# Optimization experiments

Measured on AMD Instinct MI355X. Metric: run time of the kernel, lower is better.

Reference implementation:

```python
import jax, jax.numpy as jnp
import numpy as np

D_MODEL = 2048
N_HEADS = 16
HEAD_DIM = D_MODEL // N_HEADS
B, T = 4, 2048


def setup_inputs() -> dict:
    key = jax.random.key(0)
    ks = jax.random.split(key, 10)
    s = 1.0 / np.sqrt(D_MODEL)
    x = jax.random.normal(ks[0], (B, T, D_MODEL), dtype=jnp.float32)
    # causal additive mask, broadcastable to [B, H, T, T]
    neg = jnp.finfo(jnp.float32).min
    causal = jnp.triu(jnp.full((T, T), neg, dtype=jnp.float32), k=1)
    mask = causal[None, None, :, :]
    return {
        "x": x,
        "mask": mask,
        "Wq": jax.random.uniform(ks[1], (D_MODEL, D_MODEL), jnp.float32, -s, s),
        "bq": jax.random.uniform(ks[2], (D_MODEL,), jnp.float32, -s, s),
        "Wk": jax.random.uniform(ks[3], (D_MODEL, HEAD_DIM), jnp.float32, -s, s),
        "bk": jax.random.uniform(ks[4], (HEAD_DIM,), jnp.float32, -s, s),
        "Wv": jax.random.uniform(ks[5], (D_MODEL, HEAD_DIM), jnp.float32, -s, s),
        "bv": jax.random.uniform(ks[6], (HEAD_DIM,), jnp.float32, -s, s),
        "Wo": jax.random.uniform(ks[7], (D_MODEL, D_MODEL), jnp.float32, -s, s),
        "bo": jax.random.uniform(ks[8], (D_MODEL,), jnp.float32, -s, s),
    }


def reference(x, mask, Wq, bq, Wk, bk, Wv, bv, Wo, bo):
    Bb, Tt, _ = x.shape
    H, Dh = N_HEADS, HEAD_DIM
    scale = 1.0 / jnp.sqrt(jnp.float32(Dh))
    q = (x @ Wq + bq).reshape(Bb, Tt, H, Dh)          # [B,T,H,D]
    k = x @ Wk + bk                                    # [B,T,D] (single KV head)
    v = x @ Wv + bv                                    # [B,T,D]
    # scores: [B,H,T,T] — q heads against shared k
    attn = jnp.einsum("bthd,bsd->bhts", q, k) * scale
    attn = attn + mask
    attn = jax.nn.softmax(attn, axis=-1)
    out = jnp.einsum("bhts,bsd->bthd", attn, v).reshape(Bb, Tt, D_MODEL)
    return out @ Wo + bo
```

## Files before the change

### kernel.cpp

```cpp
#include <hip/hip_runtime.h>
#include <hip/hip_bf16.h>
#include <stdint.h>

#define DEV __device__ __forceinline__

typedef unsigned short u16;
typedef unsigned int u32;
typedef __bf16 bf16x8 __attribute__((ext_vector_type(8)));
typedef float f32x4 __attribute__((ext_vector_type(4)));
typedef u16 u16x4 __attribute__((ext_vector_type(4)));
typedef u32 u32x2 __attribute__((ext_vector_type(2)));
typedef u32 u32x4 __attribute__((ext_vector_type(4)));

typedef __attribute__((address_space(1))) u32 u32_as1;
typedef __attribute__((address_space(3))) u32 u32_as3;

static constexpr int Bn = 4, Tn = 2048, Dm = 2048, Hn = 16, Dh = 128;
static constexpr int BT = Bn * Tn;
static constexpr int KVSTR = 256;

#define VMCNT(n) asm volatile("s_waitcnt vmcnt(" #n ")" ::: "memory")
#define BARRIER() __builtin_amdgcn_s_barrier()

DEV u16 f2bf(float f) {
  u32 u = __builtin_bit_cast(u32, f);
  u += 0x7fffu + ((u >> 16) & 1u);
  return (u16)(u >> 16);
}
DEV u16 cvt_bf(float f) { return __builtin_bit_cast(u16, (__bf16)f); }
DEV u32 cvt_pk_bf16(float lo, float hi) {
  u32 r;
  asm("v_cvt_pk_bf16_f32 %0, %1, %2" : "=v"(r) : "v"(lo), "v"(hi));
  return r;
}

DEV void gl2lds16(const void* g, void* l) {
  __builtin_amdgcn_global_load_lds((u32_as1*)(uintptr_t)g,
                                   (u32_as3*)(u32)(uintptr_t)l, 16, 0, 0);
}

__global__ __launch_bounds__(256) void k_cast_bf16(const float* __restrict__ in,
                                                   u16* __restrict__ out, int n4) {
  int i = blockIdx.x * 256 + threadIdx.x;
  int stride = gridDim.x * 256;
  for (; i < n4; i += stride) {
    f32x4 v = ((const f32x4*)in)[i];
    u16x4 o;
    o.x = f2bf(v.x); o.y = f2bf(v.y); o.z = f2bf(v.z); o.w = f2bf(v.w);
    ((u16x4*)out)[i] = o;
  }
}

__global__ __launch_bounds__(256) void k_transpose_cast(const float* __restrict__ in,
                                                        u16* __restrict__ out,
                                                        int R, int C) {
  __shared__ float t[32][33];
  const int r0 = blockIdx.y * 32, c0 = blockIdx.x * 32;
  const int x = threadIdx.x, y = threadIdx.y;
#pragma unroll
  for (int i = 0; i < 4; ++i)
    t[y + i * 8][x] = in[(size_t)(r0 + y + i * 8) * C + c0 + x];
  __syncthreads();
#pragma unroll
  for (int i = 0; i < 4; ++i)
    out[(size_t)(c0 + y + i * 8) * R + r0 + x] = f2bf(t[x][y + i * 8]);
}

__global__ __launch_bounds__(256) void k_transpose_bf16(const u16* __restrict__ in,
                                                        int inStride,
                                                        u16* __restrict__ out,
                                                        int R, int C) {
  __shared__ u16 t[32][34];
  const int r0 = blockIdx.y * 32, c0 = blockIdx.x * 32;
  const int x = threadIdx.x, y = threadIdx.y;
#pragma unroll
  for (int i = 0; i < 4; ++i)
    t[y + i * 8][x] = in[(size_t)(r0 + y + i * 8) * inStride + c0 + x];
  __syncthreads();
#pragma unroll
  for (int i = 0; i < 4; ++i)
    out[(size_t)(c0 + y + i * 8) * R + r0 + x] = t[x][y + i * 8];
}

__global__ void k_concat_bias(const float* __restrict__ a, const float* __restrict__ b,
                              float* __restrict__ dst) {
  int i = threadIdx.x;
  dst[i] = (i < 128) ? a[i] : b[i - 128];
}

template <typename OutT>
__global__ __launch_bounds__(256) void k_gemm_bt(const u16* __restrict__ A,
                                                 const u16* __restrict__ Bt,
                                                 const float* __restrict__ bias,
                                                 OutT* __restrict__ C,
                                                 int M, int N, int K) {
  __shared__ __align__(128) char smem[32768];
  char* As = smem;
  char* Bs = smem + 16384;
  const int tid = threadIdx.x;
  const int wid = tid >> 6, lane = tid & 63;
  const int g = lane >> 4, r = lane & 15;
  const int wr = wid >> 1, wc = wid & 1;
  const int m0 = blockIdx.x * 128, n0 = blockIdx.y * 128;

  f32x4 acc[4][4];
#pragma unroll
  for (int m = 0; m < 4; ++m)
#pragma unroll
    for (int n = 0; n < 4; ++n) acc[m][n] = (f32x4)(0.f);

  for (int k0 = 0; k0 < K; k0 += 64) {
#pragma unroll
    for (int n = 0; n < 4; ++n) {
      const int L = n * 4096 + tid * 16;
      const int row = L >> 7;
      const int colb = (L & 127) ^ ((row & 7) << 4);
      gl2lds16((const char*)A + ((size_t)(m0 + row) * K + k0) * 2 + colb, As + L);
      gl2lds16((const char*)Bt + ((size_t)(n0 + row) * K + k0) * 2 + colb, Bs + L);
    }
    __syncthreads();
#pragma unroll
    for (int kk = 0; kk < 2; ++kk) {
      bf16x8 a[4], b[4];
#pragma unroll
      for (int m = 0; m < 4; ++m) {
        const int row = wr * 64 + m * 16 + r;
        a[m] = *(const bf16x8*)(As + row * 128 + ((kk * 64 + g * 16) ^ ((row & 7) << 4)));
      }
#pragma unroll
      for (int n = 0; n < 4; ++n) {
        const int row = wc * 64 + n * 16 + r;
        b[n] = *(const bf16x8*)(Bs + row * 128 + ((kk * 64 + g * 16) ^ ((row & 7) << 4)));
      }
#pragma unroll
      for (int m = 0; m < 4; ++m)
#pragma unroll
        for (int n = 0; n < 4; ++n)
          acc[m][n] = __builtin_amdgcn_mfma_f32_16x16x32_bf16(a[m], b[n], acc[m][n], 0, 0, 0);
    }
    __syncthreads();
  }

#pragma unroll
  for (int n = 0; n < 4; ++n) {
    const int col = n0 + wc * 64 + n * 16 + r;
    const float bv = bias[col];
#pragma unroll
    for (int m = 0; m < 4; ++m) {
#pragma unroll
      for (int j = 0; j < 4; ++j) {
        const int grow = m0 + wr * 64 + m * 16 + 4 * g + j;
        const float v = acc[m][n][j] + bv;
        if constexpr (sizeof(OutT) == 2)
          ((u16*)C)[(size_t)grow * N + col] = f2bf(v);
        else
          ((float*)C)[(size_t)grow * N + col] = v;
      }
    }
  }
}

template <typename OutT>
__global__ __launch_bounds__(512, 2) void k_gemm256(const u16* __restrict__ A,
                                                    const u16* __restrict__ Bt,
                                                    const float* __restrict__ bias,
                                                    OutT* __restrict__ C,
                                                    int M, int N, int K) {
  extern __shared__ char smem[];
  const int tid = threadIdx.x;
  const int wid = tid >> 6, lane = tid & 63;
  const int g = lane >> 4, r = lane & 15;
  const int wm = wid >> 2, wn = wid & 3;

  const int nbn = N >> 8;
  const int cpx = gridDim.x >> 3;
  const int linear = (blockIdx.x & 7) * cpx + (blockIdx.x >> 3);
  const int m0 = (linear / nbn) << 8;
  const int n0 = (linear % nbn) << 8;

  const int rowInCh = lane >> 3;
  const int colb = ((lane & 7) << 4) ^ (rowInCh << 4);
  const char* srcA0; const char* srcA1; const char* srcA2; const char* srcA3;
  const char* srcB0; const char* srcB1; const char* srcB2; const char* srcB3;
  int ldsA[4], ldsB[4];
  {
    const int wnh = (wid >> 1) & 1;
    const int cbb = ((wid >> 2) << 1) | (wid & 1);
    const char* sa[4]; const char* sb[4];
#pragma unroll
    for (int i = 0; i < 4; ++i) {
      const int chA = ((wid & 3) << 2) + i;
      const int lrA = (wm << 7) + (chA << 3) + rowInCh;
      sa[i] = (const char*)A + ((size_t)(m0 + lrA) * K) * 2 + colb;
      ldsA[i] = ((wm << 7) + (chA << 3)) * 128 + lane * 16;
      const int chB = (cbb << 2) + i;
      const int lrB = (wnh << 7) + (chB << 3) + rowInCh;
      sb[i] = (const char*)Bt + ((size_t)(n0 + lrB) * K) * 2 + colb;
      ldsB[i] = 32768 + ((wnh << 7) + (chB << 3)) * 128 + lane * 16;
    }
    srcA0 = sa[0]; srcA1 = sa[1]; srcA2 = sa[2]; srcA3 = sa[3];
    srcB0 = sb[0]; srcB1 = sb[1]; srcB2 = sb[2]; srcB3 = sb[3];
  }

  auto stage = [&](int t, int b) {
    const size_t ko = (size_t)t * 128;
    char* base = smem + (b << 16);
    gl2lds16(srcA0 + ko, base + ldsA[0]);
    gl2lds16(srcA1 + ko, base + ldsA[1]);
    gl2lds16(srcA2 + ko, base + ldsA[2]);
    gl2lds16(srcA3 + ko, base + ldsA[3]);
    gl2lds16(srcB0 + ko, base + ldsB[0]);
    gl2lds16(srcB1 + ko, base + ldsB[1]);
    gl2lds16(srcB2 + ko, base + ldsB[2]);
    gl2lds16(srcB3 + ko, base + ldsB[3]);
  };

  f32x4 acc[8][4];
#pragma unroll
  for (int m = 0; m < 8; ++m)
#pragma unroll
    for (int n = 0; n < 4; ++n) acc[m][n] = (f32x4)(0.f);

  auto readA = [&](const char* Ab, int qm, bf16x8 (&a)[8]) {
#pragma unroll
    for (int m = 0; m < 4; ++m) {
      const int row = (wm << 7) + ((qm * 4 + m) << 4) + r;
#pragma unroll
      for (int kk = 0; kk < 2; ++kk)
        a[m * 2 + kk] = *(const bf16x8*)(Ab + row * 128 + ((kk * 64 + g * 16) ^ ((row & 7) << 4)));
    }
  };
  auto readB = [&](const char* Bb, int qn, bf16x8 (&b)[4]) {
#pragma unroll
    for (int n = 0; n < 2; ++n) {
      const int row = (wn << 6) + ((qn * 2 + n) << 4) + r;
#pragma unroll
      for (int kk = 0; kk < 2; ++kk)
        b[n * 2 + kk] = *(const bf16x8*)(Bb + row * 128 + ((kk * 64 + g * 16) ^ ((row & 7) << 4)));
    }
  };
  auto mfmaQ = [&](const bf16x8 (&a)[8], const bf16x8 (&b)[4], int qm, int qn) {
    __builtin_amdgcn_s_setprio(1);
#pragma unroll
    for (int m = 0; m < 4; ++m)
#pragma unroll
      for (int n = 0; n < 2; ++n)
#pragma unroll
        for (int kk = 0; kk < 2; ++kk)
          acc[qm * 4 + m][qn * 2 + n] = __builtin_amdgcn_mfma_f32_16x16x32_bf16(
              a[m * 2 + kk], b[n * 2 + kk], acc[qm * 4 + m][qn * 2 + n], 0, 0, 0);
    __builtin_amdgcn_s_setprio(0);
  };

  const int NT = K >> 6;
  stage(0, 0);
  stage(1, 1);
  VMCNT(8);
  BARRIER();

  bf16x8 a0[8], a1[8], b0[4], b1[4];
  for (int t = 0; t < NT; ++t) {
    const char* Ab = smem + ((t & 1) << 16);
    const char* Bb = Ab + 32768;
    readA(Ab, 0, a0);
    readB(Bb, 0, b0);
    BARRIER();
    mfmaQ(a0, b0, 0, 0);
    BARRIER();
    readB(Bb, 1, b1);
    BARRIER();
    mfmaQ(a0, b1, 0, 1);
    BARRIER();
    readA(Ab, 1, a1);
    BARRIER();
    mfmaQ(a1, b1, 1, 1);
    BARRIER();
    if (t + 2 < NT) {
      stage(t + 2, t & 1);
      mfmaQ(a1, b0, 1, 0);
      VMCNT(8);
    } else {
      mfmaQ(a1, b0, 1, 0);
      VMCNT(0);
    }
    BARRIER();
  }

#pragma unroll
  for (int n = 0; n < 4; ++n) {
    const int col = n0 + wn * 64 + n * 16 + r;
    const float bv = bias[col];
#pragma unroll
    for (int m = 0; m < 8; ++m) {
#pragma unroll
      for (int j = 0; j < 4; ++j) {
        const int grow = m0 + wm * 128 + m * 16 + 4 * g + j;
        const float v = acc[m][n][j] + bv;
        if constexpr (sizeof(OutT) == 2)
          ((u16*)C)[(size_t)grow * N + col] = cvt_bf(v);
        else
          ((float*)C)[(size_t)grow * N + col] = v;
      }
    }
  }
}

__global__ __launch_bounds__(256, 2) void k_attn(const u16* __restrict__ Q,
                                                 const u16* __restrict__ Kb,
                                                 const u16* __restrict__ VT,
                                                 u16* __restrict__ O) {
  __shared__ __align__(1024) char smem[49152];
  char* Vs = smem + 32768;

  const int tid = threadIdx.x;
  const int wq = tid >> 6, lane = tid & 63;
  const int g = lane >> 4, r = lane & 15;

  const int bid = blockIdx.x;
  const int xcd = bid & 7, ii = bid >> 3;
  const int b = xcd >> 1;
  const int h = ((xcd & 1) << 3) | (ii >> 3);
  const int p = ii & 7;
  const int qtA = p, qtB = 15 - p;
  const int nstA = 2 * qtA + 2;
  const int ntot = nstA + 2 * qtB + 2;

  const float cl2 = 0.1275174147f;
  const float DEFER = 62.736f;

  bf16x8 qf[2][4];
  f32x4 o[2][8];
  float mrow[2], lrow[2];

  auto loadQ = [&](int qrow0) {
#pragma unroll
    for (int m2 = 0; m2 < 2; ++m2)
#pragma unroll
      for (int c = 0; c < 4; ++c)
        qf[m2][c] = *(const bf16x8*)(Q + (size_t)(qrow0 + m2 * 16 + r) * Dm + h * Dh + c * 32 + g * 8);
  };
  auto resetAcc = [&]() {
#pragma unroll
    for (int m2 = 0; m2 < 2; ++m2) {
#pragma unroll
      for (int c = 0; c < 8; ++c) o[m2][c] = (f32x4)(0.f);
      mrow[m2] = -1e30f; lrow[m2] = 0.f;
    }
  };
  auto storeO = [&](int qrow0) {
#pragma unroll
    for (int m2 = 0; m2 < 2; ++m2) {
      float linv[4];
#pragma unroll
      for (int j = 0; j < 4; ++j)
        linv[j] = __builtin_amdgcn_rcpf(__shfl(lrow[m2], 20 * g + j));
#pragma unroll
      for (int c = 0; c < 8; ++c)
#pragma unroll
        for (int j = 0; j < 4; ++j)
          O[(size_t)(qrow0 + m2 * 16 + 4 * g + j) * Dm + h * Dh + c * 16 + r] =
              cvt_bf(o[m2][c][j] * linv[j]);
    }
  };
  auto stageK = [&](int s0, char* dst) {
#pragma unroll
    for (int n = 0; n < 4; ++n) {
      const int L = n * 4096 + tid * 16;
      const int row = L >> 8;
      const int colb = (L & 255) ^ ((row & 7) << 4);
      gl2lds16((const char*)Kb + (size_t)(s0 + row) * (KVSTR * 2) + colb, dst + L);
    }
  };
  auto stageV = [&](int s0) {
#pragma unroll
    for (int n = 0; n < 4; ++n) {
      const int L = n * 4096 + tid * 16;
      const int row = L >> 7;
      const int colb = (L & 127) ^ ((row & 7) << 4);
      gl2lds16((const char*)VT + ((size_t)row * BT + s0) * 2 + colb, Vs + L);
    }
  };

  int qt = qtA;
  int qrow0 = b * Tn + qt * 128 + wq * 32;
  int qmin = qt * 128 + wq * 32;
  loadQ(qrow0);
  resetAcc();
  stageK(b * Tn, smem);
  VMCNT(0);
  BARRIER();

  int cur = 0;
  for (int t = 0; t < ntot; ++t) {
    if (t == nstA) {
      storeO(qrow0);
      qt = qtB;
      qrow0 = b * Tn + qt * 128 + wq * 32;
      qmin = qt * 128 + wq * 32;
      loadQ(qrow0);
      resetAcc();
    }
    const int st = (t < nstA) ? t : t - nstA;
    const int s0 = b * Tn + st * 64;

    stageV(s0);
    {
      const int t1 = t + 1;
      const int st1 = (t1 >= ntot) ? 0 : ((t1 < nstA) ? t1 : t1 - nstA);
      stageK(b * Tn + st1 * 64, smem + ((cur ^ 1) << 14));
    }

    const bool fullmask = (st * 64 >= qmin + 32);
    u32x4 pau[2][2];
    if (!fullmask) {
      const char* Kc = smem + (cur << 14);
      f32x4 sf[2][4];
      __builtin_amdgcn_s_setprio(1);
#pragma unroll
      for (int n = 0; n < 4; ++n) {
        f32x4 sa = (f32x4)(0.f), sb = (f32x4)(0.f);
#pragma unroll
        for (int c = 0; c < 4; ++c) {
          const int row = n * 16 + r;
          bf16x8 kf = *(const bf16x8*)(Kc + row * 256 + ((c * 64 + g * 16) ^ ((row & 7) << 4)));
          sa = __builtin_amdgcn_mfma_f32_16x16x32_bf16(kf, qf[0][c], sa, 0, 0, 0);
          sb = __builtin_amdgcn_mfma_f32_16x16x32_bf16(kf, qf[1][c], sb, 0, 0, 0);
        }
        sf[0][n] = sa; sf[1][n] = sb;
      }
      __builtin_amdgcn_s_setprio(0);
      if (st * 64 + 63 > qmin) {
#pragma unroll
        for (int m2 = 0; m2 < 2; ++m2) {
          const int q = qmin + m2 * 16 + r;
#pragma unroll
          for (int n = 0; n < 4; ++n)
#pragma unroll
            for (int j = 0; j < 4; ++j) {
              const int key = st * 64 + n * 16 + 4 * g + j;
              if (key > q) sf[m2][n][j] = -1e30f;
            }
        }
      }
      float vmax[2];
      bool need = false;
#pragma unroll
      for (int m2 = 0; m2 < 2; ++m2) {
        f32x4 t4;
#pragma unroll
        for (int j = 0; j < 4; ++j)
          t4[j] = fmaxf(fmaxf(sf[m2][0][j], sf[m2][1][j]), fmaxf(sf[m2][2][j], sf[m2][3][j]));
        float v = fmaxf(fmaxf(t4[0], t4[1]), fmaxf(t4[2], t4[3]));
        v = fmaxf(v, __shfl_xor(v, 16));
        v = fmaxf(v, __shfl_xor(v, 32));
        vmax[m2] = v;
        need = need || (v > mrow[m2] + DEFER);
      }
      if (__any(need)) {
#pragma unroll
        for (int m2 = 0; m2 < 2; ++m2) {
          const float mnew = fmaxf(mrow[m2], vmax[m2]);
          const float fac = __builtin_amdgcn_exp2f((mrow[m2] - mnew) * cl2);
          mrow[m2] = mnew;
          lrow[m2] *= fac;
#pragma unroll
          for (int j = 0; j < 4; ++j) {
            const float fb = __shfl(fac, 20 * g + j);
#pragma unroll
            for (int c = 0; c < 8; ++c) o[m2][c][j] *= fb;
          }
        }
      }
      float rs[2] = {0.f, 0.f};
#pragma unroll
      for (int m2 = 0; m2 < 2; ++m2) {
#pragma unroll
        for (int n = 0; n < 4; ++n) {
          const float p0 = __builtin_amdgcn_exp2f((sf[m2][n][0] - mrow[m2]) * cl2);
          const float p1 = __builtin_amdgcn_exp2f((sf[m2][n][1] - mrow[m2]) * cl2);
          const float p2 = __builtin_amdgcn_exp2f((sf[m2][n][2] - mrow[m2]) * cl2);
          const float p3 = __builtin_amdgcn_exp2f((sf[m2][n][3] - mrow[m2]) * cl2);
          rs[m2] += (p0 + p1) + (p2 + p3);
          pau[m2][n >> 1][(n & 1) * 2]     = cvt_pk_bf16(p0, p1);
          pau[m2][n >> 1][(n & 1) * 2 + 1] = cvt_pk_bf16(p2, p3);
        }
        float v = rs[m2];
        v += __shfl_xor(v, 16);
        v += __shfl_xor(v, 32);
        lrow[m2] += v;
      }
    }

    VMCNT(4);
    BARRIER();

    if (!fullmask) {
      __builtin_amdgcn_s_setprio(1);
#pragma unroll
      for (int kk = 0; kk < 2; ++kk) {
        if (st * 64 + kk * 32 >= qmin + 32) continue;
        const bf16x8 pa0 = __builtin_bit_cast(bf16x8, pau[0][kk]);
        const bf16x8 pa1 = __builtin_bit_cast(bf16x8, pau[1][kk]);
#pragma unroll
        for (int c = 0; c < 8; ++c) {
          const int row = c * 16 + r;
          const int swz = (row & 7) << 4;
          const u32x2 lo = *(const u32x2*)(Vs + row * 128 + ((kk * 64 + 8 * g) ^ swz));
          const u32x2 hi = *(const u32x2*)(Vs + row * 128 + ((kk * 64 + 32 + 8 * g) ^ swz));
          u32x4 vbu;
          vbu.x = lo.x; vbu.y = lo.y; vbu.z = hi.x; vbu.w = hi.y;
          const bf16x8 vb = __builtin_bit_cast(bf16x8, vbu);
          o[0][c] = __builtin_amdgcn_mfma_f32_16x16x32_bf16(pa0, vb, o[0][c], 0, 0, 0);
          o[1][c] = __builtin_amdgcn_mfma_f32_16x16x32_bf16(pa1, vb, o[1][c], 0, 0, 0);
        }
      }
      __builtin_amdgcn_s_setprio(0);
    }

    VMCNT(0);
    BARRIER();
    cur ^= 1;
  }
  storeO(qrow0);
}

extern "C" void kernel_launch(void* const* d_in, const int* in_sizes, int n_in,
                              void* d_out, int out_size, void* d_ws, size_t ws_size,
                              hipStream_t stream) {
  const float* x  = (const float*)d_in[0];
  const float* Wq = (const float*)d_in[2];
  const float* bq = (const float*)d_in[3];
  const float* Wk = (const float*)d_in[4];
  const float* bk = (const float*)d_in[5];
  const float* Wv = (const float*)d_in[6];
  const float* bv = (const float*)d_in[7];
  const float* Wo = (const float*)d_in[8];
  const float* bo = (const float*)d_in[9];
  float* out = (float*)d_out;

  char* ws = (char*)d_ws;
  size_t off = 0;
  auto alloc = [&](size_t bytes) {
    char* p = ws + off;
    off += (bytes + 255) & ~(size_t)255;
    return p;
  };
  u16* xb   = (u16*)alloc((size_t)BT * Dm * 2);
  u16* Qb   = (u16*)alloc((size_t)BT * Dm * 2);
  u16* KVb  = (u16*)alloc((size_t)BT * KVSTR * 2);
  u16* VTb  = (u16*)alloc((size_t)BT * Dh * 2);
  u16* Wqt  = (u16*)alloc((size_t)Dm * Dm * 2);
  u16* Wkvt = (u16*)alloc((size_t)Dm * KVSTR * 2);
  u16* Wot  = (u16*)alloc((size_t)Dm * Dm * 2);
  float* bkv = (float*)alloc(KVSTR * sizeof(float));
  u16* Ob   = xb;

  hipFuncSetAttribute(reinterpret_cast<const void*>(&k_gemm256<u16>),
                      hipFuncAttributeMaxDynamicSharedMemorySize, 131072);
  hipFuncSetAttribute(reinterpret_cast<const void*>(&k_gemm256<float>),
                      hipFuncAttributeMaxDynamicSharedMemorySize, 131072);

  k_cast_bf16<<<2048, 256, 0, stream>>>(x, xb, BT * Dm / 4);
  dim3 tb(32, 8);
  k_transpose_cast<<<dim3(Dm / 32, Dm / 32), tb, 0, stream>>>(Wq, Wqt, Dm, Dm);
  k_transpose_cast<<<dim3(Dh / 32, Dm / 32), tb, 0, stream>>>(Wk, Wkvt, Dm, Dh);
  k_transpose_cast<<<dim3(Dh / 32, Dm / 32), tb, 0, stream>>>(Wv, Wkvt + (size_t)Dh * Dm, Dm, Dh);
  k_transpose_cast<<<dim3(Dm / 32, Dm / 32), tb, 0, stream>>>(Wo, Wot, Dm, Dm);
  k_concat_bias<<<1, 256, 0, stream>>>(bk, bv, bkv);

  k_gemm256<u16><<<(BT / 256) * (Dm / 256), 512, 131072, stream>>>(xb, Wqt, bq, Qb, BT, Dm, Dm);
  k_gemm_bt<u16><<<dim3(BT / 128, KVSTR / 128), 256, 0, stream>>>(xb, Wkvt, bkv, KVb, BT, KVSTR, Dm);
  k_transpose_bf16<<<dim3(Dh / 32, BT / 32), tb, 0, stream>>>(KVb + Dh, KVSTR, VTb, BT, Dh);

  k_attn<<<512, 256, 0, stream>>>(Qb, KVb, VTb, Ob);

  k_gemm256<float><<<(BT / 256) * (Dm / 256), 512, 131072, stream>>>(Ob, Wot, bo, out, BT, Dm, Dm);
}
```

Baseline: 311.0 us.

## Split attention tiles per block, fold softmax scale into Q, vectorize V loads

The attention kernel no longer pairs two query tiles (p and 15-p) per block. It launches 1024 blocks with one query tile each and raises launch bounds to 3 waves/SIMD for occupancy, giving up the explicit causal load balancing. The softmax scale times log2(e) is folded into the Q projection epilogue, which removes per-element multiplies before exp2. The V transpose permutes columns so each lane can read a single 16-byte LDS vector instead of two 8-byte loads, and the max reductions use v_max3.

```diff
diff --git a/kernel.cpp b/kernel.cpp
--- a/kernel.cpp
+++ b/kernel.cpp
@@ -9,7 +9,6 @@
 typedef __bf16 bf16x8 __attribute__((ext_vector_type(8)));
 typedef float f32x4 __attribute__((ext_vector_type(4)));
 typedef u16 u16x4 __attribute__((ext_vector_type(4)));
-typedef u32 u32x2 __attribute__((ext_vector_type(2)));
 typedef u32 u32x4 __attribute__((ext_vector_type(4)));
 
 typedef __attribute__((address_space(1))) u32 u32_as1;
@@ -18,6 +17,7 @@
 static constexpr int Bn = 4, Tn = 2048, Dm = 2048, Hn = 16, Dh = 128;
 static constexpr int BT = Bn * Tn;
 static constexpr int KVSTR = 256;
+static constexpr float CL2 = 0.1275174147f;
 
 #define VMCNT(n) asm volatile("s_waitcnt vmcnt(" #n ")" ::: "memory")
 #define BARRIER() __builtin_amdgcn_s_barrier()
@@ -32,6 +32,11 @@
   u32 r;
   asm("v_cvt_pk_bf16_f32 %0, %1, %2" : "=v"(r) : "v"(lo), "v"(hi));
   return r;
+}
+DEV float max3f(float a, float b, float c) {
+  float d;
+  asm("v_max3_f32 %0, %1, %2, %3" : "=v"(d) : "v"(a), "v"(b), "v"(c));
+  return d;
 }
 
 DEV void gl2lds16(const void* g, void* l) {
@@ -66,10 +71,10 @@
     out[(size_t)(c0 + y + i * 8) * R + r0 + x] = f2bf(t[x][y + i * 8]);
 }
 
-__global__ __launch_bounds__(256) void k_transpose_bf16(const u16* __restrict__ in,
-                                                        int inStride,
-                                                        u16* __restrict__ out,
-                                                        int R, int C) {
+__global__ __launch_bounds__(256) void k_transpose_v(const u16* __restrict__ in,
+                                                     int inStride,
+                                                     u16* __restrict__ out,
+                                                     int R, int C) {
   __shared__ u16 t[32][34];
   const int r0 = blockIdx.y * 32, c0 = blockIdx.x * 32;
   const int x = threadIdx.x, y = threadIdx.y;
@@ -77,9 +82,10 @@
   for (int i = 0; i < 4; ++i)
     t[y + i * 8][x] = in[(size_t)(r0 + y + i * 8) * inStride + c0 + x];
   __syncthreads();
+  const int sx = (((x & 7) >> 2) << 4) | (((x >> 3) & 3) << 2) | (x & 3);
 #pragma unroll
   for (int i = 0; i < 4; ++i)
-    out[(size_t)(c0 + y + i * 8) * R + r0 + x] = t[x][y + i * 8];
+    out[(size_t)(c0 + y + i * 8) * R + r0 + x] = t[sx][y + i * 8];
 }
 
 __global__ void k_concat_bias(const float* __restrict__ a, const float* __restrict__ b,
@@ -165,7 +171,8 @@
                                                     const u16* __restrict__ Bt,
                                                     const float* __restrict__ bias,
                                                     OutT* __restrict__ C,
-                                                    int M, int N, int K) {
+                                                    int M, int N, int K,
+                                                    float oscale) {
   extern __shared__ char smem[];
   const int tid = threadIdx.x;
   const int wid = tid >> 6, lane = tid & 63;
@@ -295,7 +302,7 @@
 #pragma unroll
       for (int j = 0; j < 4; ++j) {
         const int grow = m0 + wm * 128 + m * 16 + 4 * g + j;
-        const float v = acc[m][n][j] + bv;
+        const float v = (acc[m][n][j] + bv) * oscale;
         if constexpr (sizeof(OutT) == 2)
           ((u16*)C)[(size_t)grow * N + col] = cvt_bf(v);
         else
@@ -305,7 +312,7 @@
   }
 }
 
-__global__ __launch_bounds__(256, 2) void k_attn(const u16* __restrict__ Q,
+__global__ __launch_bounds__(256, 3) void k_attn(const u16* __restrict__ Q,
                                                  const u16* __restrict__ Kb,
                                                  const u16* __restrict__ VT,
                                                  u16* __restrict__ O) {
@@ -319,49 +326,29 @@
   const int bid = blockIdx.x;
   const int xcd = bid & 7, ii = bid >> 3;
   const int b = xcd >> 1;
-  const int h = ((xcd & 1) << 3) | (ii >> 3);
-  const int p = ii & 7;
-  const int qtA = p, qtB = 15 - p;
-  const int nstA = 2 * qtA + 2;
-  const int ntot = nstA + 2 * qtB + 2;
-
-  const float cl2 = 0.1275174147f;
-  const float DEFER = 62.736f;
+  const int h = ((xcd & 1) << 3) | (ii & 7);
+  const int qt = 15 - (ii >> 3);
+  const int ntot = 2 * qt + 2;
+
+  const float DEFER = 8.0f;
 
   bf16x8 qf[2][4];
   f32x4 o[2][8];
   float mrow[2], lrow[2];
 
-  auto loadQ = [&](int qrow0) {
-#pragma unroll
-    for (int m2 = 0; m2 < 2; ++m2)
-#pragma unroll
-      for (int c = 0; c < 4; ++c)
-        qf[m2][c] = *(const bf16x8*)(Q + (size_t)(qrow0 + m2 * 16 + r) * Dm + h * Dh + c * 32 + g * 8);
-  };
-  auto resetAcc = [&]() {
-#pragma unroll
-    for (int m2 = 0; m2 < 2; ++m2) {
-#pragma unroll
-      for (int c = 0; c < 8; ++c) o[m2][c] = (f32x4)(0.f);
-      mrow[m2] = -1e30f; lrow[m2] = 0.f;
-    }
-  };
-  auto storeO = [&](int qrow0) {
-#pragma unroll
-    for (int m2 = 0; m2 < 2; ++m2) {
-      float linv[4];
-#pragma unroll
-      for (int j = 0; j < 4; ++j)
-        linv[j] = __builtin_amdgcn_rcpf(__shfl(lrow[m2], 20 * g + j));
-#pragma unroll
-      for (int c = 0; c < 8; ++c)
-#pragma unroll
-        for (int j = 0; j < 4; ++j)
-          O[(size_t)(qrow0 + m2 * 16 + 4 * g + j) * Dm + h * Dh + c * 16 + r] =
-              cvt_bf(o[m2][c][j] * linv[j]);
-    }
-  };
+  const int qrow0 = b * Tn + qt * 128 + wq * 32;
+  const int qmin = qt * 128 + wq * 32;
+
+#pragma unroll
+  for (int m2 = 0; m2 < 2; ++m2) {
+#pragma unroll
+    for (int c = 0; c < 4; ++c)
+      qf[m2][c] = *(const bf16x8*)(Q + (size_t)(qrow0 + m2 * 16 + r) * Dm + h * Dh + c * 32 + g * 8);
+#pragma unroll
+    for (int c = 0; c < 8; ++c) o[m2][c] = (f32x4)(0.f);
+    mrow[m2] = -1e30f; lrow[m2] = 0.f;
+  }
+
   auto stageK = [&](int s0, char* dst) {
 #pragma unroll
     for (int n = 0; n < 4; ++n) {
@@ -381,36 +368,21 @@
     }
   };
 
-  int qt = qtA;
-  int qrow0 = b * Tn + qt * 128 + wq * 32;
-  int qmin = qt * 128 + wq * 32;
-  loadQ(qrow0);
-  resetAcc();
   stageK(b * Tn, smem);
   VMCNT(0);
   BARRIER();
 
   int cur = 0;
   for (int t = 0; t < ntot; ++t) {
-    if (t == nstA) {
-      storeO(qrow0);
-      qt = qtB;
-      qrow0 = b * Tn + qt * 128 + wq * 32;
-      qmin = qt * 128 + wq * 32;
-      loadQ(qrow0);
-      resetAcc();
-    }
-    const int st = (t < nstA) ? t : t - nstA;
-    const int s0 = b * Tn + st * 64;
+    const int s0 = b * Tn + t * 64;
 
     stageV(s0);
     {
-      const int t1 = t + 1;
-      const int st1 = (t1 >= ntot) ? 0 : ((t1 < nstA) ? t1 : t1 - nstA);
+      const int st1 = (t + 1 < ntot) ? t + 1 : 0;
       stageK(b * Tn + st1 * 64, smem + ((cur ^ 1) << 14));
     }
 
-    const bool fullmask = (st * 64 >= qmin + 32);
+    const bool fullmask = (t * 64 >= qmin + 32);
     u32x4 pau[2][2];
     if (!fullmask) {
       const char* Kc = smem + (cur << 14);
@@ -429,7 +401,7 @@
         sf[0][n] = sa; sf[1][n] = sb;
       }
       __builtin_amdgcn_s_setprio(0);
-      if (st * 64 + 63 > qmin) {
+      if (t * 64 + 63 > qmin) {
 #pragma unroll
         for (int m2 = 0; m2 < 2; ++m2) {
           const int q = qmin + m2 * 16 + r;
@@ -437,7 +409,7 @@
           for (int n = 0; n < 4; ++n)
 #pragma unroll
             for (int j = 0; j < 4; ++j) {
-              const int key = st * 64 + n * 16 + 4 * g + j;
+              const int key = t * 64 + n * 16 + 4 * g + j;
               if (key > q) sf[m2][n][j] = -1e30f;
             }
         }
@@ -449,8 +421,8 @@
         f32x4 t4;
 #pragma unroll
         for (int j = 0; j < 4; ++j)
-          t4[j] = fmaxf(fmaxf(sf[m2][0][j], sf[m2][1][j]), fmaxf(sf[m2][2][j], sf[m2][3][j]));
-        float v = fmaxf(fmaxf(t4[0], t4[1]), fmaxf(t4[2], t4[3]));
+          t4[j] = fmaxf(max3f(sf[m2][0][j], sf[m2][1][j], sf[m2][2][j]), sf[m2][3][j]);
+        float v = fmaxf(max3f(t4[0], t4[1], t4[2]), t4[3]);
         v = fmaxf(v, __shfl_xor(v, 16));
         v = fmaxf(v, __shfl_xor(v, 32));
         vmax[m2] = v;
@@ -460,7 +432,7 @@
 #pragma unroll
         for (int m2 = 0; m2 < 2; ++m2) {
           const float mnew = fmaxf(mrow[m2], vmax[m2]);
-          const float fac = __builtin_amdgcn_exp2f((mrow[m2] - mnew) * cl2);
+          const float fac = __builtin_amdgcn_exp2f(mrow[m2] - mnew);
           mrow[m2] = mnew;
           lrow[m2] *= fac;
 #pragma unroll
@@ -471,23 +443,22 @@
           }
         }
       }
-      float rs[2] = {0.f, 0.f};
 #pragma unroll
       for (int m2 = 0; m2 < 2; ++m2) {
+        float rs = 0.f;
 #pragma unroll
         for (int n = 0; n < 4; ++n) {
-          const float p0 = __builtin_amdgcn_exp2f((sf[m2][n][0] - mrow[m2]) * cl2);
-          const float p1 = __builtin_amdgcn_exp2f((sf[m2][n][1] - mrow[m2]) * cl2);
-          const float p2 = __builtin_amdgcn_exp2f((sf[m2][n][2] - mrow[m2]) * cl2);
-          const float p3 = __builtin_amdgcn_exp2f((sf[m2][n][3] - mrow[m2]) * cl2);
-          rs[m2] += (p0 + p1) + (p2 + p3);
+          const float p0 = __builtin_amdgcn_exp2f(sf[m2][n][0] - mrow[m2]);
+          const float p1 = __builtin_amdgcn_exp2f(sf[m2][n][1] - mrow[m2]);
+          const float p2 = __builtin_amdgcn_exp2f(sf[m2][n][2] - mrow[m2]);
+          const float p3 = __builtin_amdgcn_exp2f(sf[m2][n][3] - mrow[m2]);
+          rs += (p0 + p1) + (p2 + p3);
           pau[m2][n >> 1][(n & 1) * 2]     = cvt_pk_bf16(p0, p1);
           pau[m2][n >> 1][(n & 1) * 2 + 1] = cvt_pk_bf16(p2, p3);
         }
-        float v = rs[m2];
-        v += __shfl_xor(v, 16);
-        v += __shfl_xor(v, 32);
-        lrow[m2] += v;
+        rs += __shfl_xor(rs, 16);
+        rs += __shfl_xor(rs, 32);
+        lrow[m2] += rs;
       }
     }
 
@@ -498,18 +469,13 @@
       __builtin_amdgcn_s_setprio(1);
 #pragma unroll
       for (int kk = 0; kk < 2; ++kk) {
-        if (st * 64 + kk * 32 >= qmin + 32) continue;
+        if (t * 64 + kk * 32 >= qmin + 32) continue;
         const bf16x8 pa0 = __builtin_bit_cast(bf16x8, pau[0][kk]);
         const bf16x8 pa1 = __builtin_bit_cast(bf16x8, pau[1][kk]);
 #pragma unroll
         for (int c = 0; c < 8; ++c) {
           const int row = c * 16 + r;
-          const int swz = (row & 7) << 4;
-          const u32x2 lo = *(const u32x2*)(Vs + row * 128 + ((kk * 64 + 8 * g) ^ swz));
-          const u32x2 hi = *(const u32x2*)(Vs + row * 128 + ((kk * 64 + 32 + 8 * g) ^ swz));
-          u32x4 vbu;
-          vbu.x = lo.x; vbu.y = lo.y; vbu.z = hi.x; vbu.w = hi.y;
-          const bf16x8 vb = __builtin_bit_cast(bf16x8, vbu);
+          const bf16x8 vb = *(const bf16x8*)(Vs + row * 128 + ((kk * 64 + g * 16) ^ ((row & 7) << 4)));
           o[0][c] = __builtin_amdgcn_mfma_f32_16x16x32_bf16(pa0, vb, o[0][c], 0, 0, 0);
           o[1][c] = __builtin_amdgcn_mfma_f32_16x16x32_bf16(pa1, vb, o[1][c], 0, 0, 0);
         }
@@ -521,7 +487,20 @@
     BARRIER();
     cur ^= 1;
   }
-  storeO(qrow0);
+
+#pragma unroll
+  for (int m2 = 0; m2 < 2; ++m2) {
+    float linv[4];
+#pragma unroll
+    for (int j = 0; j < 4; ++j)
+      linv[j] = __builtin_amdgcn_rcpf(__shfl(lrow[m2], 20 * g + j));
+#pragma unroll
+    for (int c = 0; c < 8; ++c)
+#pragma unroll
+      for (int j = 0; j < 4; ++j)
+        O[(size_t)(qrow0 + m2 * 16 + 4 * g + j) * Dm + h * Dh + c * 16 + r] =
+            cvt_bf(o[m2][c][j] * linv[j]);
+  }
 }
 
 extern "C" void kernel_launch(void* const* d_in, const int* in_sizes, int n_in,
@@ -568,11 +547,11 @@
   k_transpose_cast<<<dim3(Dm / 32, Dm / 32), tb, 0, stream>>>(Wo, Wot, Dm, Dm);
   k_concat_bias<<<1, 256, 0, stream>>>(bk, bv, bkv);
 
-  k_gemm256<u16><<<(BT / 256) * (Dm / 256), 512, 131072, stream>>>(xb, Wqt, bq, Qb, BT, Dm, Dm);
+  k_gemm256<u16><<<(BT / 256) * (Dm / 256), 512, 131072, stream>>>(xb, Wqt, bq, Qb, BT, Dm, Dm, CL2);
   k_gemm_bt<u16><<<dim3(BT / 128, KVSTR / 128), 256, 0, stream>>>(xb, Wkvt, bkv, KVb, BT, KVSTR, Dm);
-  k_transpose_bf16<<<dim3(Dh / 32, BT / 32), tb, 0, stream>>>(KVb + Dh, KVSTR, VTb, BT, Dh);
-
-  k_attn<<<512, 256, 0, stream>>>(Qb, KVb, VTb, Ob);
-
-  k_gemm256<float><<<(BT / 256) * (Dm / 256), 512, 131072, stream>>>(Ob, Wot, bo, out, BT, Dm, Dm);
-}
+  k_transpose_v<<<dim3(Dh / 32, BT / 32), tb, 0, stream>>>(KVb + Dh, KVSTR, VTb, BT, Dh);
+
+  k_attn<<<1024, 256, 0, stream>>>(Qb, KVb, VTb, Ob);
+
+  k_gemm256<float><<<(BT / 256) * (Dm / 256), 512, 131072, stream>>>(Ob, Wot, bo, out, BT, Dm, Dm, 1.0f);
+}
```

After: 326.6 us. 5.0% more time.
